# Optimization experiments

Measured on AMD Instinct MI355X. Metric: run time of the kernel, lower is better.

The kernel has to match this reference:

```python
import jax, jax.numpy as jnp
import numpy as np

N = 100000   # nodes
E = 1600000  # edges
P = 16       # num_properties
H = 64       # hidden_dim
EPS = 1e-12  # F.normalize eps


def _lin_params(key, din, dout):
    return (jax.random.normal(key, (din, dout), jnp.float32) / np.sqrt(din),
            jnp.zeros((dout,), jnp.float32))


def _mlp(x, W1, b1, W2, b2):
    # MLP(in, out, hidden_layers=[H]): Linear -> ReLU -> Linear
    return jnp.maximum(x @ W1 + b1, 0.0) @ W2 + b2


def setup_inputs() -> dict:
    key = jax.random.key(0)
    ks = jax.random.split(key, 12)
    h = jax.random.normal(ks[0], (N, P), jnp.float32)
    x = jax.random.normal(ks[1], (N, 3), jnp.float32)
    edge_index = jax.random.randint(ks[2], (2, E), 0, N, jnp.int64)
    emb_W, emb_b = _lin_params(ks[3], P, H)
    eW1, eb1 = _lin_params(ks[4], 2 * H + 1, H)
    eW2, eb2 = _lin_params(ks[5], H, H)
    nW1, nb1 = _lin_params(ks[6], 2 * H, H)
    nW2, nb2 = _lin_params(ks[7], H, H)
    wW1, wb1 = _lin_params(ks[8], H, H)
    wW2, wb2 = _lin_params(ks[9], H, 1)
    return {"h": h, "x": x, "edge_index": edge_index,
            "emb_W": emb_W, "emb_b": emb_b,
            "eW1": eW1, "eb1": eb1, "eW2": eW2, "eb2": eb2,
            "nW1": nW1, "nb1": nb1, "nW2": nW2, "nb2": nb2,
            "wW1": wW1, "wb1": wb1, "wW2": wW2, "wb2": wb2}


def reference(h, x, edge_index, emb_W, emb_b, eW1, eb1, eW2, eb2,
              nW1, nb1, nW2, nb2, wW1, wb1, wW2, wb2):
    row, col = edge_index[0], edge_index[1]
    h = h @ emb_W + emb_b  # [N,H] node embedding

    rel_pos = x[row] - x[col]                               # [E,3]
    rel_dist = jnp.sum(rel_pos ** 2, axis=-1, keepdims=True)  # [E,1]
    rel_theta = jnp.arctan2(rel_pos[:, 1], rel_pos[:, 0])
    rel_phi = jnp.arctan2(rel_pos[:, 2],
                          jnp.sqrt(rel_pos[:, 0] ** 2 + rel_pos[:, 1] ** 2))
    rel_pos_spin2 = rel_dist * jnp.stack(
        [jnp.cos(2 * rel_theta), jnp.sin(2 * rel_theta), rel_phi], axis=1)  # [E,3]

    # single layer (num_layers=1; original code only executable in this config)
    edge_inputs = jnp.concatenate([h[row], h[col], rel_dist], axis=-1)  # [E,2H+1]
    edge_feat = _mlp(edge_inputs, eW1, eb1, eW2, eb2)                   # [E,H]
    agg = jax.ops.segment_sum(edge_feat, row, num_segments=N)           # [N,H]
    h = h + _mlp(jnp.concatenate([h, agg], axis=-1), nW1, nb1, nW2, nb2)

    w = _mlp(edge_feat, wW1, wb1, wW2, wb2)              # [E,1]
    rel_scaled = rel_pos_spin2[:, None, :] * w[:, :, None]  # [E,1,3]
    v_sum = jax.ops.segment_sum(rel_scaled, row, num_segments=N)  # [N,1,3]
    cnt = jax.ops.segment_sum(jnp.ones((E,), jnp.float32), row, num_segments=N)
    v = v_sum / jnp.maximum(cnt, 1.0)[:, None, None]     # scatter-mean

    v = v[:, :2]  # slice along dim 1 (faithful to torch v[:, :2])
    norm = jnp.linalg.norm(v, axis=-1, keepdims=True)
    v = v / jnp.maximum(norm, EPS)  # F.normalize(p=2, dim=-1)
    return (h, x, v)
```

## Files before the change

kernel.cpp:

```cpp
#include <hip/hip_runtime.h>
#include <math.h>

#define NN 100000
#define EE 1600000
#define NBLK_SCAN 256
#define CHUNK ((NN + NBLK_SCAN - 1) / NBLK_SCAN)

typedef __attribute__((ext_vector_type(8))) short bf16x8;
typedef __attribute__((ext_vector_type(4))) float f32x4;

__device__ __forceinline__ ushort f2bf(float x) {
    uint u = __builtin_bit_cast(uint, x);
    u += 0x7fffu + ((u >> 16) & 1u);
    return (ushort)(u >> 16);
}
__device__ __forceinline__ float bf2f(ushort u) {
    uint v = ((uint)u) << 16;
    return __builtin_bit_cast(float, v);
}

__global__ __launch_bounds__(256) void embed_kernel(
    const float* __restrict__ h, const float* __restrict__ embW,
    const float* __restrict__ embB, ushort* __restrict__ hembb)
{
    int t = blockIdx.x * 256 + threadIdx.x;
    int n = t >> 6;
    int j = t & 63;
    if (n >= NN) return;
    float acc = embB[j];
#pragma unroll
    for (int k = 0; k < 16; ++k)
        acc = fmaf(h[n * 16 + k], embW[k * 64 + j], acc);
    hembb[n * 64 + j] = f2bf(acc);
}

__global__ __launch_bounds__(256) void hist_kernel(
    const int* __restrict__ ei, int* __restrict__ hist)
{
    for (int e = blockIdx.x * 256 + threadIdx.x; e < EE; e += gridDim.x * 256)
        atomicAdd(&hist[ei[e]], 1);
}

__global__ __launch_bounds__(256) void scan_a(const int* __restrict__ hist, int* __restrict__ bsum)
{
    __shared__ int red[256];
    const int b = blockIdx.x, t = threadIdx.x;
    const int start = b * CHUNK, end = min(NN, start + CHUNK);
    int s = 0;
    for (int i = start + t; i < end; i += 256) s += hist[i];
    red[t] = s; __syncthreads();
    for (int k = 128; k > 0; k >>= 1) { if (t < k) red[t] += red[t + k]; __syncthreads(); }
    if (t == 0) bsum[b] = red[0];
}

__global__ void scan_b(const int* __restrict__ bsum, int* __restrict__ boff)
{
    if (threadIdx.x == 0) {
        int acc = 0;
        for (int i = 0; i < NBLK_SCAN; ++i) { boff[i] = acc; acc += bsum[i]; }
    }
}

__global__ __launch_bounds__(256) void scan_c(
    const int* __restrict__ hist, const int* __restrict__ boff,
    int* __restrict__ csr, int* __restrict__ cursor)
{
    __shared__ int lds[CHUNK];
    const int b = blockIdx.x, t = threadIdx.x;
    const int start = b * CHUNK, end = min(NN, start + CHUNK), n = end - start;
    for (int i = t; i < n; i += 256) lds[i] = hist[start + i];
    __syncthreads();
    if (t == 0) {
        int acc = boff[b];
        for (int i = 0; i < n; ++i) { int v = lds[i]; lds[i] = acc; acc += v; }
        if (end == NN) csr[NN] = acc;
    }
    __syncthreads();
    for (int i = t; i < n; i += 256) { csr[start + i] = lds[i]; cursor[start + i] = lds[i]; }
}

__global__ __launch_bounds__(256) void scatter_kernel(
    const int* __restrict__ ei, int* __restrict__ cursor, int2* __restrict__ srt)
{
    for (int e = blockIdx.x * 256 + threadIdx.x; e < EE; e += gridDim.x * 256) {
        const int row = ei[e];
        const int p = atomicAdd(&cursor[row], 1);
        srt[p] = make_int2(row, ei[EE + e]);
    }
}

__global__ __launch_bounds__(512, 2) void edge_kernel(
    const ushort* __restrict__ hembb, const float* __restrict__ x,
    const int2* __restrict__ srt,
    const float* __restrict__ eW1, const float* __restrict__ eb1,
    const float* __restrict__ eW2, const float* __restrict__ eb2,
    const float* __restrict__ wW1, const float* __restrict__ wb1,
    const float* __restrict__ wW2, const float* __restrict__ wb2,
    float* __restrict__ agg, float* __restrict__ vsum)
{
    __shared__ ushort sWB[32 * 512];
    __shared__ ushort sS[8][1280];
    __shared__ float  sScal[8][16][4];

    const int tid = threadIdx.x;
    const int wave = tid >> 6, lane = tid & 63;
    const int l15 = lane & 15, g = lane >> 4;

#pragma unroll
    for (int q = 0; q < 2; ++q) {
        const int fi = wave * 2 + q;
        const int kc = fi >> 2, t = fi & 3;
        bf16x8 f;
#pragma unroll
        for (int b = 0; b < 8; ++b)
            f[b] = (short)f2bf(eW1[(kc * 32 + g * 8 + b) * 64 + t * 16 + l15]);
        *(bf16x8*)&sWB[fi * 512 + lane * 8] = f;
    }
    {
        const int kc = wave >> 2, t = wave & 3;
        bf16x8 f, fv;
#pragma unroll
        for (int b = 0; b < 8; ++b) {
            int s = kc * 32 + g * 8 + b;
            int j = (s >> 2) + (s & 3) * 16;
            f[b]  = (short)f2bf(eW2[j * 64 + t * 16 + l15]);
            fv[b] = (short)f2bf(wW1[j * 64 + t * 16 + l15]);
        }
        *(bf16x8*)&sWB[(16 + wave) * 512 + lane * 8] = f;
        *(bf16x8*)&sWB[(24 + wave) * 512 + lane * 8] = fv;
    }

    float b1v[4], b2v[4], wb1v[4], w2v[4], w128v[4];
#pragma unroll
    for (int t = 0; t < 4; ++t) {
        b1v[t]   = eb1[t * 16 + l15];
        b2v[t]   = eb2[t * 16 + l15];
        wb1v[t]  = wb1[t * 16 + l15];
        w2v[t]   = wW2[t * 16 + l15];
        w128v[t] = eW1[128 * 64 + t * 16 + l15];
    }
    const float wb2v = wb2[0];
    __syncthreads();

    ushort* SC = sS[wave];

    const int base = (blockIdx.x * 8 + wave) * 400;

    float carry = 0.f, carryv = 0.f;
    int cur_row = -1;

    for (int bt = 0; bt < 25; ++bt) {
        const int ebase = base + bt * 16;

        int rowv = 0, colv = 0;
        if (lane < 16) {
            const int2 rc = srt[ebase + lane];
            rowv = rc.x; colv = rc.y;
            const float dx = x[rowv * 3 + 0] - x[colv * 3 + 0];
            const float dy = x[rowv * 3 + 1] - x[colv * 3 + 1];
            const float dz = x[rowv * 3 + 2] - x[colv * 3 + 2];
            const float r2 = dx * dx + dy * dy;
            const float rdv = r2 + dz * dz;
            const float inv = (r2 > 0.f) ? (1.f / r2) : 0.f;
            const float c2  = (r2 > 0.f) ? ((dx * dx - dy * dy) * inv) : 1.f;
            const float sn2 = 2.f * dx * dy * inv;
            const float phi = atan2f(dz, sqrtf(r2));
            float4 sc = {rdv, rdv * c2, rdv * sn2, rdv * phi};
            *(float4*)&sScal[wave][lane][0] = sc;
        }

        const int rowN = __shfl(rowv, l15);
        const int colN = __shfl(colv, l15);
        const bf16x8 a0 = *(const bf16x8*)&hembb[(size_t)rowN * 64 + g * 8];
        const bf16x8 a1 = *(const bf16x8*)&hembb[(size_t)rowN * 64 + 32 + g * 8];
        const bf16x8 a2 = *(const bf16x8*)&hembb[(size_t)colN * 64 + g * 8];
        const bf16x8 a3 = *(const bf16x8*)&hembb[(size_t)colN * 64 + 32 + g * 8];

        f32x4 acc[4];
#pragma unroll
        for (int t = 0; t < 4; ++t) acc[t] = (f32x4){b1v[t], b1v[t], b1v[t], b1v[t]};
#pragma unroll
        for (int t = 0; t < 4; ++t) {
            acc[t] = __builtin_amdgcn_mfma_f32_16x16x32_bf16(
                a0, *(const bf16x8*)&sWB[(0 * 4 + t) * 512 + lane * 8], acc[t], 0, 0, 0);
            acc[t] = __builtin_amdgcn_mfma_f32_16x16x32_bf16(
                a1, *(const bf16x8*)&sWB[(1 * 4 + t) * 512 + lane * 8], acc[t], 0, 0, 0);
            acc[t] = __builtin_amdgcn_mfma_f32_16x16x32_bf16(
                a2, *(const bf16x8*)&sWB[(2 * 4 + t) * 512 + lane * 8], acc[t], 0, 0, 0);
            acc[t] = __builtin_amdgcn_mfma_f32_16x16x32_bf16(
                a3, *(const bf16x8*)&sWB[(3 * 4 + t) * 512 + lane * 8], acc[t], 0, 0, 0);
        }
#pragma unroll
        for (int r = 0; r < 4; ++r) {
            const float rd_r = sScal[wave][g * 4 + r][0];
#pragma unroll
            for (int t = 0; t < 4; ++t) acc[t][r] = fmaf(rd_r, w128v[t], acc[t][r]);
        }
#pragma unroll
        for (int r = 0; r < 4; ++r) {
            const float v0 = fmaxf(acc[0][r], 0.f), v1 = fmaxf(acc[1][r], 0.f);
            const float v2 = fmaxf(acc[2][r], 0.f), v3 = fmaxf(acc[3][r], 0.f);
            uint2 p;
            p.x = (uint)f2bf(v0) | ((uint)f2bf(v1) << 16);
            p.y = (uint)f2bf(v2) | ((uint)f2bf(v3) << 16);
            *(uint2*)&SC[(g * 4 + r) * 80 + l15 * 4] = p;
        }

        f32x4 acc2[4];
#pragma unroll
        for (int t = 0; t < 4; ++t) acc2[t] = (f32x4){b2v[t], b2v[t], b2v[t], b2v[t]};
#pragma unroll
        for (int kc = 0; kc < 2; ++kc) {
            bf16x8 a = *(const bf16x8*)&SC[l15 * 80 + kc * 32 + g * 8];
#pragma unroll
            for (int t = 0; t < 4; ++t)
                acc2[t] = __builtin_amdgcn_mfma_f32_16x16x32_bf16(
                    a, *(const bf16x8*)&sWB[(16 + kc * 4 + t) * 512 + lane * 8], acc2[t], 0, 0, 0);
        }
#pragma unroll
        for (int r = 0; r < 4; ++r) {
            uint2 p;
            p.x = (uint)f2bf(acc2[0][r]) | ((uint)f2bf(acc2[1][r]) << 16);
            p.y = (uint)f2bf(acc2[2][r]) | ((uint)f2bf(acc2[3][r]) << 16);
            *(uint2*)&SC[(g * 4 + r) * 80 + l15 * 4] = p;
        }

        f32x4 acc3[4];
#pragma unroll
        for (int t = 0; t < 4; ++t) acc3[t] = (f32x4){wb1v[t], wb1v[t], wb1v[t], wb1v[t]};
#pragma unroll
        for (int kc = 0; kc < 2; ++kc) {
            bf16x8 a = *(const bf16x8*)&SC[l15 * 80 + kc * 32 + g * 8];
#pragma unroll
            for (int t = 0; t < 4; ++t)
                acc3[t] = __builtin_amdgcn_mfma_f32_16x16x32_bf16(
                    a, *(const bf16x8*)&sWB[(24 + kc * 4 + t) * 512 + lane * 8], acc3[t], 0, 0, 0);
        }
        float wfin[4];
#pragma unroll
        for (int r = 0; r < 4; ++r) {
            float p = fmaxf(acc3[0][r], 0.f) * w2v[0];
            p = fmaf(fmaxf(acc3[1][r], 0.f), w2v[1], p);
            p = fmaf(fmaxf(acc3[2][r], 0.f), w2v[2], p);
            p = fmaf(fmaxf(acc3[3][r], 0.f), w2v[3], p);
            wfin[r] = p;
        }
#pragma unroll
        for (int m = 1; m < 16; m <<= 1) {
#pragma unroll
            for (int r = 0; r < 4; ++r) wfin[r] += __shfl_xor(wfin[r], m);
        }
#pragma unroll
        for (int r = 0; r < 4; ++r) wfin[r] += wb2v;

#pragma unroll
        for (int e = 0; e < 16; ++e) {
            const int row_e = __shfl(rowv, e);
            const float efv = bf2f(SC[e * 80 + l15 * 4 + g]);
            const float wE = __shfl(wfin[e & 3], (e >> 2) * 16);
            if (row_e != cur_row) {
                if (cur_row >= 0) {
                    unsafeAtomicAdd(&agg[(size_t)cur_row * 64 + lane], carry);
                    if (lane < 3) unsafeAtomicAdd(&vsum[cur_row * 4 + lane], carryv);
                }
                cur_row = row_e; carry = 0.f; carryv = 0.f;
            }
            carry += efv;
            if (lane < 3) carryv = fmaf(sScal[wave][e][1 + lane], wE, carryv);
        }
    }
    if (cur_row >= 0) {
        unsafeAtomicAdd(&agg[(size_t)cur_row * 64 + lane], carry);
        if (lane < 3) unsafeAtomicAdd(&vsum[cur_row * 4 + lane], carryv);
    }
}

__global__ __launch_bounds__(256, 2) void node_kernel(
    const ushort* __restrict__ hembb, const float* __restrict__ agg,
    const float* __restrict__ nW1, const float* __restrict__ nb1,
    const float* __restrict__ nW2, const float* __restrict__ nb2,
    const float* __restrict__ vsum, const int* __restrict__ csr,
    float* __restrict__ outh, float* __restrict__ outv)
{
    __shared__ ushort sT1[4][16 * 80];

    const int tid = threadIdx.x;
    const int wave = tid >> 6, lane = tid & 63;
    const int l15 = lane & 15, g = lane >> 4;

    bf16x8 W1f[4][4], W2f[2][4];
#pragma unroll
    for (int kc = 0; kc < 4; ++kc)
#pragma unroll
        for (int t = 0; t < 4; ++t) {
            bf16x8 f;
#pragma unroll
            for (int b = 0; b < 8; ++b) {
                int k = kc * 32 + g * 8 + b;
                f[b] = (short)f2bf(nW1[k * 64 + t * 16 + l15]);
            }
            W1f[kc][t] = f;
        }
#pragma unroll
    for (int kc = 0; kc < 2; ++kc)
#pragma unroll
        for (int t = 0; t < 4; ++t) {
            bf16x8 f;
#pragma unroll
            for (int b = 0; b < 8; ++b) {
                int s = kc * 32 + g * 8 + b;
                int j = (s >> 2) + (s & 3) * 16;
                f[b] = (short)f2bf(nW2[j * 64 + t * 16 + l15]);
            }
            W2f[kc][t] = f;
        }
    float b1v[4], b2v[4];
#pragma unroll
    for (int t = 0; t < 4; ++t) { b1v[t] = nb1[t * 16 + l15]; b2v[t] = nb2[t * 16 + l15]; }

    ushort* T1 = sT1[wave];
    const int nwaves = gridDim.x * 4;
    const int ntiles = NN / 16;

    for (int tile = blockIdx.x * 4 + wave; tile < ntiles; tile += nwaves) {
        const int nb = tile * 16;

        f32x4 acc[4];
#pragma unroll
        for (int t = 0; t < 4; ++t) acc[t] = (f32x4){b1v[t], b1v[t], b1v[t], b1v[t]};
#pragma unroll
        for (int kc = 0; kc < 2; ++kc) {
            bf16x8 a = *(const bf16x8*)&hembb[(size_t)(nb + l15) * 64 + kc * 32 + g * 8];
#pragma unroll
            for (int t = 0; t < 4; ++t)
                acc[t] = __builtin_amdgcn_mfma_f32_16x16x32_bf16(a, W1f[kc][t], acc[t], 0, 0, 0);
        }
#pragma unroll
        for (int kc = 2; kc < 4; ++kc) {
            const float4 f0 = *(const float4*)&agg[(size_t)(nb + l15) * 64 + (kc - 2) * 32 + g * 8];
            const float4 f1 = *(const float4*)&agg[(size_t)(nb + l15) * 64 + (kc - 2) * 32 + g * 8 + 4];
            bf16x8 a;
            a[0] = (short)f2bf(f0.x); a[1] = (short)f2bf(f0.y);
            a[2] = (short)f2bf(f0.z); a[3] = (short)f2bf(f0.w);
            a[4] = (short)f2bf(f1.x); a[5] = (short)f2bf(f1.y);
            a[6] = (short)f2bf(f1.z); a[7] = (short)f2bf(f1.w);
#pragma unroll
            for (int t = 0; t < 4; ++t)
                acc[t] = __builtin_amdgcn_mfma_f32_16x16x32_bf16(a, W1f[kc][t], acc[t], 0, 0, 0);
        }
#pragma unroll
        for (int r = 0; r < 4; ++r) {
            const float v0 = fmaxf(acc[0][r], 0.f), v1 = fmaxf(acc[1][r], 0.f);
            const float v2 = fmaxf(acc[2][r], 0.f), v3 = fmaxf(acc[3][r], 0.f);
            uint2 p;
            p.x = (uint)f2bf(v0) | ((uint)f2bf(v1) << 16);
            p.y = (uint)f2bf(v2) | ((uint)f2bf(v3) << 16);
            *(uint2*)&T1[(g * 4 + r) * 80 + l15 * 4] = p;
        }

        f32x4 acc2[4];
#pragma unroll
        for (int t = 0; t < 4; ++t) acc2[t] = (f32x4){b2v[t], b2v[t], b2v[t], b2v[t]};
#pragma unroll
        for (int kc = 0; kc < 2; ++kc) {
            bf16x8 a = *(const bf16x8*)&T1[l15 * 80 + kc * 32 + g * 8];
#pragma unroll
            for (int t = 0; t < 4; ++t)
                acc2[t] = __builtin_amdgcn_mfma_f32_16x16x32_bf16(a, W2f[kc][t], acc2[t], 0, 0, 0);
        }
#pragma unroll
        for (int r = 0; r < 4; ++r) {
#pragma unroll
            for (int t = 0; t < 4; ++t) {
                const size_t idx = (size_t)(nb + g * 4 + r) * 64 + t * 16 + l15;
                outh[idx] = bf2f(hembb[idx]) + acc2[t][r];
            }
        }

        if (g == 0) {
            const int n = nb + l15;
            const float c = fmaxf((float)(csr[n + 1] - csr[n]), 1.f);
            const float4 vs = *(const float4*)&vsum[n * 4];
            const float a0 = vs.x / c, a1 = vs.y / c, a2 = vs.z / c;
            const float nrm = fmaxf(sqrtf(a0 * a0 + a1 * a1 + a2 * a2), 1e-12f);
            outv[n * 3 + 0] = a0 / nrm;
            outv[n * 3 + 1] = a1 / nrm;
            outv[n * 3 + 2] = a2 / nrm;
        }
    }
}

extern "C" void kernel_launch(void* const* d_in, const int* in_sizes, int n_in,
                              void* d_out, int out_size, void* d_ws, size_t ws_size,
                              hipStream_t stream)
{
    const float* h    = (const float*)d_in[0];
    const float* x    = (const float*)d_in[1];
    const int*   ei   = (const int*)d_in[2];
    const float* embW = (const float*)d_in[3];
    const float* embB = (const float*)d_in[4];
    const float* eW1  = (const float*)d_in[5];
    const float* eb1  = (const float*)d_in[6];
    const float* eW2  = (const float*)d_in[7];
    const float* eb2  = (const float*)d_in[8];
    const float* nW1  = (const float*)d_in[9];
    const float* nb1  = (const float*)d_in[10];
    const float* nW2  = (const float*)d_in[11];
    const float* nb2  = (const float*)d_in[12];
    const float* wW1  = (const float*)d_in[13];
    const float* wb1  = (const float*)d_in[14];
    const float* wW2  = (const float*)d_in[15];
    const float* wb2  = (const float*)d_in[16];

    float* ws     = (float*)d_ws;
    ushort* hembb = (ushort*)ws;
    float* agg    = ws + (size_t)NN * 32;
    float* vsum   = agg + (size_t)NN * 64;
    int*   hist   = (int*)(vsum + (size_t)NN * 4);
    int*   csr    = hist + NN;
    int*   cursor = csr + NN + 1;
    int*   bsum   = cursor + NN;
    int*   boff   = bsum + NBLK_SCAN;
    int2*  srt    = (int2*)(boff + NBLK_SCAN);

    float* outh = (float*)d_out;
    float* outx = outh + (size_t)NN * 64;
    float* outv = outx + (size_t)NN * 3;

    hipMemsetAsync(agg, 0, ((size_t)NN * 64 + NN * 4 + NN) * sizeof(float), stream);

    embed_kernel<<<NN * 64 / 256, 256, 0, stream>>>(h, embW, embB, hembb);
    hipMemcpyAsync(outx, x, (size_t)NN * 3 * sizeof(float), hipMemcpyDeviceToDevice, stream);

    hist_kernel<<<2048, 256, 0, stream>>>(ei, hist);
    scan_a<<<NBLK_SCAN, 256, 0, stream>>>(hist, bsum);
    scan_b<<<1, 64, 0, stream>>>(bsum, boff);
    scan_c<<<NBLK_SCAN, 256, 0, stream>>>(hist, boff, csr, cursor);
    scatter_kernel<<<2048, 256, 0, stream>>>(ei, cursor, srt);

    edge_kernel<<<500, 512, 0, stream>>>(hembb, x, srt, eW1, eb1, eW2, eb2,
                                         wW1, wb1, wW2, wb2, agg, vsum);
    node_kernel<<<1563, 256, 0, stream>>>(hembb, agg, nW1, nb1, nW2, nb2,
                                          vsum, csr, outh, outv);
}
```

Baseline: 477.7 us.

## Software-pipeline edge gathers and geometry across batches in edge kernel

Restructures the edge loop so the srt indices are prefetched two batches ahead. The hembb row/col gathers and x coordinates for the next batch are issued during the current batch's MLP, and its geometry scalars go into a double-buffered shared array. This hides global gather latency behind MFMA work. It costs extra registers (next-batch operands held live), which may reduce occupancy under launch_bounds(512,2), plus a redundant srt reload in the prologue.

```diff
diff --git a/kernel.cpp b/kernel.cpp
--- a/kernel.cpp
+++ b/kernel.cpp
@@ -100,7 +100,7 @@
 {
     __shared__ ushort sWB[32 * 512];
     __shared__ ushort sS[8][1280];
-    __shared__ float  sScal[8][16][4];
+    __shared__ float  sScal[8][2][16][4];
 
     const int tid = threadIdx.x;
     const int wave = tid >> 6, lane = tid & 63;
@@ -143,18 +143,16 @@
     __syncthreads();
 
     ushort* SC = sS[wave];
-
     const int base = (blockIdx.x * 8 + wave) * 400;
 
     float carry = 0.f, carryv = 0.f;
     int cur_row = -1;
 
-    for (int bt = 0; bt < 25; ++bt) {
-        const int ebase = base + bt * 16;
-
-        int rowv = 0, colv = 0;
+    int rowv = 0;
+    {
+        int colv = 0;
         if (lane < 16) {
-            const int2 rc = srt[ebase + lane];
+            const int2 rc = srt[base + lane];
             rowv = rc.x; colv = rc.y;
             const float dx = x[rowv * 3 + 0] - x[colv * 3 + 0];
             const float dy = x[rowv * 3 + 1] - x[colv * 3 + 1];
@@ -166,15 +164,31 @@
             const float sn2 = 2.f * dx * dy * inv;
             const float phi = atan2f(dz, sqrtf(r2));
             float4 sc = {rdv, rdv * c2, rdv * sn2, rdv * phi};
-            *(float4*)&sScal[wave][lane][0] = sc;
-        }
-
+            *(float4*)&sScal[wave][0][lane][0] = sc;
+        }
         const int rowN = __shfl(rowv, l15);
         const int colN = __shfl(colv, l15);
-        const bf16x8 a0 = *(const bf16x8*)&hembb[(size_t)rowN * 64 + g * 8];
-        const bf16x8 a1 = *(const bf16x8*)&hembb[(size_t)rowN * 64 + 32 + g * 8];
-        const bf16x8 a2 = *(const bf16x8*)&hembb[(size_t)colN * 64 + g * 8];
-        const bf16x8 a3 = *(const bf16x8*)&hembb[(size_t)colN * 64 + 32 + g * 8];
+        (void)rowN; (void)colN;
+    }
+    bf16x8 a0, a1, a2, a3;
+    {
+        int colv0 = 0;
+        if (lane < 16) colv0 = srt[base + lane].y;
+        const int rowN = __shfl(rowv, l15);
+        const int colN = __shfl(colv0, l15);
+        a0 = *(const bf16x8*)&hembb[(size_t)rowN * 64 + g * 8];
+        a1 = *(const bf16x8*)&hembb[(size_t)rowN * 64 + 32 + g * 8];
+        a2 = *(const bf16x8*)&hembb[(size_t)colN * 64 + g * 8];
+        a3 = *(const bf16x8*)&hembb[(size_t)colN * 64 + 32 + g * 8];
+    }
+    int2 rc2 = make_int2(0, 0);
+    if (lane < 16) rc2 = srt[min(base + 16 + lane, EE - 1)];
+
+    int buf = 0;
+
+    for (int bt = 0; bt < 25; ++bt) {
+        int2 rc3 = make_int2(0, 0);
+        if (lane < 16) rc3 = srt[min(base + (bt + 2) * 16 + lane, EE - 1)];
 
         f32x4 acc[4];
 #pragma unroll
@@ -192,7 +206,7 @@
         }
 #pragma unroll
         for (int r = 0; r < 4; ++r) {
-            const float rd_r = sScal[wave][g * 4 + r][0];
+            const float rd_r = sScal[wave][buf][g * 4 + r][0];
 #pragma unroll
             for (int t = 0; t < 4; ++t) acc[t][r] = fmaf(rd_r, w128v[t], acc[t][r]);
         }
@@ -206,6 +220,19 @@
             *(uint2*)&SC[(g * 4 + r) * 80 + l15 * 4] = p;
         }
 
+        const int rv2 = rc2.x, cv2 = rc2.y;
+        const int rowN2 = __shfl(rv2, l15);
+        const int colN2 = __shfl(cv2, l15);
+        const bf16x8 n0 = *(const bf16x8*)&hembb[(size_t)rowN2 * 64 + g * 8];
+        const bf16x8 n1 = *(const bf16x8*)&hembb[(size_t)rowN2 * 64 + 32 + g * 8];
+        const bf16x8 n2 = *(const bf16x8*)&hembb[(size_t)colN2 * 64 + g * 8];
+        const bf16x8 n3 = *(const bf16x8*)&hembb[(size_t)colN2 * 64 + 32 + g * 8];
+        float xr0 = 0.f, xr1 = 0.f, xr2 = 0.f, xc0 = 0.f, xc1 = 0.f, xc2 = 0.f;
+        if (lane < 16) {
+            xr0 = x[rv2 * 3 + 0]; xr1 = x[rv2 * 3 + 1]; xr2 = x[rv2 * 3 + 2];
+            xc0 = x[cv2 * 3 + 0]; xc1 = x[cv2 * 3 + 1]; xc2 = x[cv2 * 3 + 2];
+        }
+
         f32x4 acc2[4];
 #pragma unroll
         for (int t = 0; t < 4; ++t) acc2[t] = (f32x4){b2v[t], b2v[t], b2v[t], b2v[t]};
@@ -223,6 +250,18 @@
             p.x = (uint)f2bf(acc2[0][r]) | ((uint)f2bf(acc2[1][r]) << 16);
             p.y = (uint)f2bf(acc2[2][r]) | ((uint)f2bf(acc2[3][r]) << 16);
             *(uint2*)&SC[(g * 4 + r) * 80 + l15 * 4] = p;
+        }
+
+        if (lane < 16) {
+            const float dx = xr0 - xc0, dy = xr1 - xc1, dz = xr2 - xc2;
+            const float r2 = dx * dx + dy * dy;
+            const float rdv = r2 + dz * dz;
+            const float inv = (r2 > 0.f) ? (1.f / r2) : 0.f;
+            const float c2  = (r2 > 0.f) ? ((dx * dx - dy * dy) * inv) : 1.f;
+            const float sn2 = 2.f * dx * dy * inv;
+            const float phi = atan2f(dz, sqrtf(r2));
+            float4 sc = {rdv, rdv * c2, rdv * sn2, rdv * phi};
+            *(float4*)&sScal[wave][buf ^ 1][lane][0] = sc;
         }
 
         f32x4 acc3[4];
@@ -266,8 +305,13 @@
                 cur_row = row_e; carry = 0.f; carryv = 0.f;
             }
             carry += efv;
-            if (lane < 3) carryv = fmaf(sScal[wave][e][1 + lane], wE, carryv);
-        }
+            if (lane < 3) carryv = fmaf(sScal[wave][buf][e][1 + lane], wE, carryv);
+        }
+
+        rowv = rv2;
+        a0 = n0; a1 = n1; a2 = n2; a3 = n3;
+        rc2 = rc3;
+        buf ^= 1;
     }
     if (cur_row >= 0) {
         unsafeAtomicAdd(&agg[(size_t)cur_row * 64 + lane], carry);
```

After: 456.1 us. -4.5%, faster.
